# Kernel optimization log

Hardware: AMD Instinct MI355X
Metric: run time of the kernel (lower is better)

## Reference

```python
import jax, jax.numpy as jnp
import numpy as np

B, S, HID = 2, 2048, 3072
NH, NKV, HD = 16, 8, 256
N_REP = NH // NKV
BITS, BLK = 4, 128
THETA = 10000.0
NEG = -1e9


def quantize_bfp(x, bits=BITS, block_size=BLK):
    """Block-floating-point quantization: blocks of `block_size` along the last
    (head_dim) axis share one power-of-two exponent; mantissas get `bits` levels
    (sign + bits-1), round-to-nearest."""
    shape = x.shape
    xb = x.reshape(-1, block_size)
    maxabs = jnp.max(jnp.abs(xb), axis=-1, keepdims=True)
    e = jnp.floor(jnp.log2(jnp.maximum(maxabs, 1e-30)))
    scale = jnp.exp2(e - (bits - 2))  # largest mantissa ~ 2^(bits-1)-1 covers maxabs
    qmax = 2.0 ** (bits - 1) - 1.0
    q = jnp.clip(jnp.round(xb / scale), -qmax, qmax) * scale
    q = jnp.where(maxabs > 0, q, 0.0)
    return q.reshape(shape)


def rotate_half(x):
    x1, x2 = jnp.split(x, 2, axis=-1)
    return jnp.concatenate((-x2, x1), axis=-1)


def setup_inputs() -> dict:
    key = jax.random.key(0)
    ks = jax.random.split(key, 5)
    hidden_states = jax.random.normal(ks[0], (B, S, HID), dtype=jnp.float32)
    sd = 0.02
    Wq = jax.random.normal(ks[1], (NH * HD, HID), dtype=jnp.float32) * sd
    Wk = jax.random.normal(ks[2], (NKV * HD, HID), dtype=jnp.float32) * sd
    Wv = jax.random.normal(ks[3], (NKV * HD, HID), dtype=jnp.float32) * sd
    Wo = jax.random.normal(ks[4], (HID, NH * HD), dtype=jnp.float32) * sd
    # rotary tables (HF convention: concat(freqs, freqs))
    pos = jnp.arange(S, dtype=jnp.float32)
    inv_freq = 1.0 / (THETA ** (jnp.arange(0, HD, 2, dtype=jnp.float32) / HD))
    freqs = jnp.einsum('s,d->sd', pos, inv_freq)
    emb = jnp.concatenate((freqs, freqs), axis=-1)  # (S, HD)
    cos = jnp.cos(emb)[None]  # (1, S, HD)
    sin = jnp.sin(emb)[None]
    # additive causal mask (B, 1, S, S)
    causal = jnp.where(jnp.tril(jnp.ones((S, S), dtype=bool)), 0.0, NEG).astype(jnp.float32)
    attention_mask = jnp.broadcast_to(causal[None, None], (B, 1, S, S))
    return {"hidden_states": hidden_states, "Wq": Wq, "Wk": Wk, "Wv": Wv,
            "Wo": Wo, "cos": cos, "sin": sin, "attention_mask": attention_mask}


def reference(hidden_states, Wq, Wk, Wv, Wo, cos, sin, attention_mask):
    b, s, _ = hidden_states.shape
    q = jnp.einsum('bsh,dh->bsd', hidden_states, Wq).reshape(b, s, NH, HD).transpose(0, 2, 1, 3)
    k = jnp.einsum('bsh,dh->bsd', hidden_states, Wk).reshape(b, s, NKV, HD).transpose(0, 2, 1, 3)
    v = jnp.einsum('bsh,dh->bsd', hidden_states, Wv).reshape(b, s, NKV, HD).transpose(0, 2, 1, 3)
    # RoPE (cos/sin unsqueezed at dim 1 -> (1,1,S,HD))
    c, sn = cos[:, None], sin[:, None]
    q = q * c + rotate_half(q) * sn
    k = k * c + rotate_half(k) * sn
    # int4 BFP quantization of keys (along rows of head_dim)
    k = quantize_bfp(k)
    # GQA: repeat kv heads
    k = jnp.repeat(k, N_REP, axis=1)
    v = jnp.repeat(v, N_REP, axis=1)
    scores = jnp.einsum('bhqd,bhkd->bhqk', q, k) / jnp.sqrt(jnp.float32(HD))
    scores = scores + attention_mask
    attn = jax.nn.softmax(scores.astype(jnp.float32), axis=-1).astype(q.dtype)
    out = jnp.einsum('bhqk,bhkd->bhqd', attn, v)
    out = out.transpose(0, 2, 1, 3).reshape(b, s, NH * HD)
    return jnp.einsum('bsd,hd->bsh', out, Wo)
```

## Files before the change

kernel.cpp:

```cpp
#include <hip/hip_runtime.h>
#include <math.h>

#define Bsz 2
#define Ssz 2048
#define HIDs 3072
#define NHs 16
#define NKVs 8
#define HDs 256

typedef _Float16 f16;
typedef _Float16 f16x8 __attribute__((ext_vector_type(8)));
typedef _Float16 f16x4 __attribute__((ext_vector_type(4)));
typedef float f32x4 __attribute__((ext_vector_type(4)));

__device__ __forceinline__ void async16(const f16* g, f16* l) {
    __builtin_amdgcn_global_load_lds(
        (const __attribute__((address_space(1))) void*)g,
        (__attribute__((address_space(3))) void*)l, 16, 0, 0);
}

__device__ __forceinline__ float row_max16(float v) {
    int t;
    t = __builtin_amdgcn_mov_dpp(__float_as_int(v), 0x121, 0xf, 0xf, false);
    v = fmaxf(v, __int_as_float(t));
    t = __builtin_amdgcn_mov_dpp(__float_as_int(v), 0x122, 0xf, 0xf, false);
    v = fmaxf(v, __int_as_float(t));
    t = __builtin_amdgcn_mov_dpp(__float_as_int(v), 0x124, 0xf, 0xf, false);
    v = fmaxf(v, __int_as_float(t));
    t = __builtin_amdgcn_mov_dpp(__float_as_int(v), 0x128, 0xf, 0xf, false);
    v = fmaxf(v, __int_as_float(t));
    return v;
}
__device__ __forceinline__ float row_sum16(float v) {
    int t;
    t = __builtin_amdgcn_mov_dpp(__float_as_int(v), 0x121, 0xf, 0xf, false);
    v = v + __int_as_float(t);
    t = __builtin_amdgcn_mov_dpp(__float_as_int(v), 0x122, 0xf, 0xf, false);
    v = v + __int_as_float(t);
    t = __builtin_amdgcn_mov_dpp(__float_as_int(v), 0x124, 0xf, 0xf, false);
    v = v + __int_as_float(t);
    t = __builtin_amdgcn_mov_dpp(__float_as_int(v), 0x128, 0xf, 0xf, false);
    v = v + __int_as_float(t);
    return v;
}

__global__ void cast_f32_f16_v4(const float4* __restrict__ in, f16x4* __restrict__ out, int n4) {
    int i = blockIdx.x * blockDim.x + threadIdx.x;
    if (i < n4) {
        float4 v = in[i];
        f16x4 r;
        r[0] = (f16)v.x; r[1] = (f16)v.y; r[2] = (f16)v.z; r[3] = (f16)v.w;
        out[i] = r;
    }
}

__global__ __launch_bounds__(256) void gemm_nt_f16(
    const f16* __restrict__ A, const f16* __restrict__ Bm, float* __restrict__ C,
    int M, int N, int K)
{
    __shared__ __align__(16) f16 As[128 * 32];
    __shared__ __align__(16) f16 Bs[128 * 32];
    const int tid  = threadIdx.x;
    const int wave = tid >> 6, lane = tid & 63;
    const int l15  = lane & 15, quad = lane >> 4;
    const int m0 = blockIdx.y * 128, n0 = blockIdx.x * 128;
    const int wm = (wave >> 1) * 64, wn = (wave & 1) * 64;
    const int srow = wave * 32 + (lane >> 2);
    const int scol = (lane & 3) * 8;

    f32x4 acc[4][4];
    const f32x4 fz = {0.f, 0.f, 0.f, 0.f};
#pragma unroll
    for (int i = 0; i < 4; i++)
#pragma unroll
        for (int j = 0; j < 4; j++) acc[i][j] = fz;

    const f16* Ag0 = A  + (size_t)(m0 + srow) * K + scol;
    const f16* Ag1 = A  + (size_t)(m0 + srow + 16) * K + scol;
    const f16* Bg0 = Bm + (size_t)(n0 + srow) * K + scol;
    const f16* Bg1 = Bm + (size_t)(n0 + srow + 16) * K + scol;
    f16* Al0 = As + (wave * 32) * 32;
    f16* Al1 = As + (wave * 32 + 16) * 32;
    f16* Bl0 = Bs + (wave * 32) * 32;
    f16* Bl1 = Bs + (wave * 32 + 16) * 32;

    for (int k0 = 0; k0 < K; k0 += 32) {
        __syncthreads();
        async16(Ag0 + k0, Al0);
        async16(Ag1 + k0, Al1);
        async16(Bg0 + k0, Bl0);
        async16(Bg1 + k0, Bl1);
        __syncthreads();
        f16x8 af[4], bfr[4];
#pragma unroll
        for (int i = 0; i < 4; i++)
            af[i] = *(const f16x8*)(As + (wm + i * 16 + l15) * 32 + quad * 8);
#pragma unroll
        for (int j = 0; j < 4; j++)
            bfr[j] = *(const f16x8*)(Bs + (wn + j * 16 + l15) * 32 + quad * 8);
#pragma unroll
        for (int i = 0; i < 4; i++)
#pragma unroll
            for (int j = 0; j < 4; j++)
                acc[i][j] = __builtin_amdgcn_mfma_f32_16x16x32_f16(af[i], bfr[j], acc[i][j], 0, 0, 0);
    }
#pragma unroll
    for (int i = 0; i < 4; i++) {
        const int r = m0 + wm + i * 16 + quad * 4;
#pragma unroll
        for (int j = 0; j < 4; j++) {
            const int c = n0 + wn + j * 16 + l15;
#pragma unroll
            for (int rr = 0; rr < 4; rr++)
                C[(size_t)(r + rr) * N + c] = acc[i][j][rr];
        }
    }
}

__global__ void rope_q_kernel(const float* __restrict__ qp, const float* __restrict__ cosb,
                              const float* __restrict__ sinb, f16* __restrict__ qo) {
    const int s = blockIdx.x, h = blockIdx.y, b = blockIdx.z;
    const int d = threadIdx.x;
    const float* row = qp + (size_t)(b * Ssz + s) * (NHs * HDs) + h * HDs;
    float x = row[d];
    float other = (d < 128) ? -row[d + 128] : row[d - 128];
    float val = (x * cosb[s * HDs + d] + other * sinb[s * HDs + d]) * 0.0625f;
    qo[((size_t)(b * NHs + h) * Ssz + s) * HDs + d] = (f16)val;
}

__global__ void rope_quant_k_kernel(const float* __restrict__ kp, const float* __restrict__ cosb,
                                    const float* __restrict__ sinb, f16* __restrict__ ko) {
    const int s = blockIdx.x, h = blockIdx.y, b = blockIdx.z;
    const int d = threadIdx.x;
    const float* row = kp + (size_t)(b * Ssz + s) * (NKVs * HDs) + h * HDs;
    float x = row[d];
    float other = (d < 128) ? -row[d + 128] : row[d - 128];
    float val = x * cosb[s * HDs + d] + other * sinb[s * HDs + d];
    __shared__ float red[256];
    red[d] = fabsf(val);
    __syncthreads();
    for (int off = 64; off >= 1; off >>= 1) {
        if ((d & 127) < off) red[d] = fmaxf(red[d], red[d + off]);
        __syncthreads();
    }
    float maxabs = red[d & 128];
    float out;
    if (maxabs > 0.f) {
        int ex;
        frexpf(maxabs, &ex);
        float scale = ldexpf(1.0f, ex - 3);
        float q = rintf(val / scale);
        q = fminf(7.f, fmaxf(-7.f, q));
        out = q * scale;
    } else out = 0.f;
    ko[((size_t)(b * NKVs + h) * Ssz + s) * HDs + d] = (f16)out;
}

__global__ __launch_bounds__(256) void transpose_v_kernel(
    const float* __restrict__ proj, f16* __restrict__ vt)
{
    const int s0 = blockIdx.x * 64, c0 = blockIdx.y * 64, b = blockIdx.z;
    const int tid = threadIdx.x;
    __shared__ f16 T[64 * 72];
    {
        const int r = tid >> 2, cc = (tid & 3) * 16;
        const float* src = proj + (size_t)(b * Ssz + s0 + r) * (NKVs * HDs) + c0 + cc;
        f16 tmp[16];
#pragma unroll
        for (int q4 = 0; q4 < 4; q4++) {
            float4 v = *(const float4*)(src + q4 * 4);
            tmp[q4 * 4 + 0] = (f16)v.x; tmp[q4 * 4 + 1] = (f16)v.y;
            tmp[q4 * 4 + 2] = (f16)v.z; tmp[q4 * 4 + 3] = (f16)v.w;
        }
        *(f16x8*)(T + r * 72 + cc)     = *(f16x8*)(tmp);
        *(f16x8*)(T + r * 72 + cc + 8) = *(f16x8*)(tmp + 8);
    }
    __syncthreads();
    {
        const int d = tid >> 2, sc = (tid & 3) * 16;
        f16 tmp[16];
#pragma unroll
        for (int j = 0; j < 16; j++) tmp[j] = T[(sc + j) * 72 + d];
        const int col = c0 + d;
        const int kh = col >> 8, dd = col & 255;
        f16* dst = vt + ((size_t)(b * NKVs + kh) * HDs + dd) * Ssz + s0 + sc;
        *(f16x8*)(dst)     = *(f16x8*)(tmp);
        *(f16x8*)(dst + 8) = *(f16x8*)(tmp + 8);
    }
}

__global__ __launch_bounds__(256, 2) void attn_kernel(
    const f16* __restrict__ Q,
    const f16* __restrict__ Kq,
    const f16* __restrict__ Vt,
    f16* __restrict__ O)
{
    const int qt = (gridDim.x - 1) - blockIdx.x;
    const int h = blockIdx.y, b = blockIdx.z;
    const int kh = h >> 1;
    const int tid = threadIdx.x;
    const int wave = tid >> 6, lane = tid & 63;
    const int l15 = lane & 15, quad = lane >> 4;
    const int wrow = qt * 64 + wave * 16;

    const f16* Qb  = Q  + ((size_t)(b * NHs  + h)  * Ssz) * HDs;
    const f16* Kg  = Kq + ((size_t)(b * NKVs + kh) * Ssz) * HDs;
    const f16* Vtg = Vt + ((size_t)(b * NKVs + kh) * HDs) * Ssz;

    __shared__ __align__(16) f16 Ks[32 * 256];
    __shared__ __align__(16) f16 Vs[256 * 32];
    __shared__ __align__(16) f16 Pl[4 * 16 * 40];
    f16* Pw = Pl + wave * 16 * 40;

    const int k_r   = lane >> 5;
    const int k_cs  = (lane & 31) ^ (k_r << 2);
    const int v_r   = lane >> 2;
    const int v_c   = (lane & 3) * 8;

    f16x8 qf[8];
    {
        const f16* qrow = Qb + (size_t)(wrow + l15) * HDs + quad * 8;
#pragma unroll
        for (int ks = 0; ks < 8; ks++)
            qf[ks] = *(const f16x8*)(qrow + ks * 32);
    }

    const f32x4 fz = {0.f, 0.f, 0.f, 0.f};
    f32x4 accO[16];
#pragma unroll
    for (int jn = 0; jn < 16; jn++) accO[jn] = fz;
    float mrow[4], lpart[4];
#pragma unroll
    for (int r = 0; r < 4; r++) { mrow[r] = -1e30f; lpart[r] = 0.f; }

    const int nk = 2 * qt + 2;
    const int wave_max_row = wrow + 15;

    for (int kt = 0; kt < nk; kt++) {
        const int kvb = kt * 32;
        __syncthreads();
#pragma unroll
        for (int t = 0; t < 4; t++) {
            const int r2 = wave * 8 + t * 2;
            async16(Kg + (size_t)(kvb + r2 + k_r) * 256 + k_cs * 8, Ks + r2 * 256);
        }
#pragma unroll
        for (int t = 0; t < 4; t++) {
            const int d0 = wave * 64 + t * 16;
            async16(Vtg + (size_t)(d0 + v_r) * Ssz + kvb + v_c, Vs + d0 * 32);
        }
        __syncthreads();

        if (kvb <= wave_max_row) {
            f32x4 sv0 = fz, sv1 = fz;
            const int sw0 = (l15 & 1) << 2;
#pragma unroll
            for (int ks = 0; ks < 8; ks++) {
                const int cpos = ((ks * 4 + quad) ^ sw0) * 8;
                f16x8 kf0 = *(const f16x8*)(Ks + l15 * 256 + cpos);
                f16x8 kf1 = *(const f16x8*)(Ks + (16 + l15) * 256 + cpos);
                sv0 = __builtin_amdgcn_mfma_f32_16x16x32_f16(qf[ks], kf0, sv0, 0, 0, 0);
                sv1 = __builtin_amdgcn_mfma_f32_16x16x32_f16(qf[ks], kf1, sv1, 0, 0, 0);
            }
            float aup[4];
            bool need = false;
#pragma unroll
            for (int r = 0; r < 4; r++) {
                float s0 = sv0[r], s1 = sv1[r];
                const int row = wrow + quad * 4 + r;
                if (kvb + 31 > row) {
                    if (kvb + l15 > row)      s0 = -1e30f;
                    if (kvb + 16 + l15 > row) s1 = -1e30f;
                }
                float rmax = row_max16(fmaxf(s0, s1));
                float mold = mrow[r];
                float mnew = fmaxf(mold, rmax);
                aup[r] = __expf(mold - mnew);
                need = need || (mnew > mold);
                float p0 = __expf(s0 - mnew);
                float p1 = __expf(s1 - mnew);
                lpart[r] = lpart[r] * aup[r] + (p0 + p1);
                mrow[r] = mnew;
                Pw[(quad * 4 + r) * 40 + l15]      = (f16)p0;
                Pw[(quad * 4 + r) * 40 + 16 + l15] = (f16)p1;
            }
            if (__any(need)) {
#pragma unroll
                for (int jn = 0; jn < 16; jn++) {
                    f32x4 t = accO[jn];
                    t[0] *= aup[0]; t[1] *= aup[1]; t[2] *= aup[2]; t[3] *= aup[3];
                    accO[jn] = t;
                }
            }
            f16x8 pf = *(const f16x8*)(Pw + l15 * 40 + quad * 8);
#pragma unroll
            for (int jn = 0; jn < 16; jn++) {
                f16x8 vf = *(const f16x8*)(Vs + (jn * 16 + l15) * 32 + quad * 8);
                accO[jn] = __builtin_amdgcn_mfma_f32_16x16x32_f16(pf, vf, accO[jn], 0, 0, 0);
            }
        }
    }
#pragma unroll
    for (int r = 0; r < 4; r++) {
        const int row = wrow + quad * 4 + r;
        const float inv = 1.0f / row_sum16(lpart[r]);
        f16* orow = O + ((size_t)(b * Ssz) + row) * (NHs * HDs) + h * HDs;
#pragma unroll
        for (int jn = 0; jn < 16; jn++)
            orow[jn * 16 + l15] = (f16)(accO[jn][r] * inv);
    }
}

extern "C" void kernel_launch(void* const* d_in, const int* in_sizes, int n_in,
                              void* d_out, int out_size, void* d_ws, size_t ws_size,
                              hipStream_t stream) {
    const float* hs   = (const float*)d_in[0];
    const float* Wq   = (const float*)d_in[1];
    const float* Wk   = (const float*)d_in[2];
    const float* Wv   = (const float*)d_in[3];
    const float* Wo   = (const float*)d_in[4];
    const float* cosb = (const float*)d_in[5];
    const float* sinb = (const float*)d_in[6];
    float* out = (float*)d_out;

    char* ws = (char*)d_ws;
    f16*   hs_h = (f16*)(ws);
    f16*   w_h  = (f16*)(ws + 25165824);
    float* proj = (float*)(ws + 50331648);
    f16*   q_h  = (f16*)(ws + 117440512);
    f16*   k_h  = (f16*)(ws + 150994944);
    f16*   vt_h = (f16*)(ws + 167772160);
    f16*   ao_h = (f16*)proj;

    int n4;
    n4 = (Bsz * Ssz * HIDs) / 4;
    cast_f32_f16_v4<<<n4 / 256, 256, 0, stream>>>((const float4*)hs, (f16x4*)hs_h, n4);
    n4 = (NHs * HDs * HIDs) / 4;
    cast_f32_f16_v4<<<n4 / 256, 256, 0, stream>>>((const float4*)Wq, (f16x4*)w_h, n4);
    gemm_nt_f16<<<dim3(4096 / 128, 4096 / 128), 256, 0, stream>>>(hs_h, w_h, proj, 4096, 4096, 3072);
    rope_q_kernel<<<dim3(Ssz, NHs, Bsz), 256, 0, stream>>>(proj, cosb, sinb, q_h);
    n4 = (NKVs * HDs * HIDs) / 4;
    cast_f32_f16_v4<<<n4 / 256, 256, 0, stream>>>((const float4*)Wk, (f16x4*)w_h, n4);
    gemm_nt_f16<<<dim3(2048 / 128, 4096 / 128), 256, 0, stream>>>(hs_h, w_h, proj, 4096, 2048, 3072);
    rope_quant_k_kernel<<<dim3(Ssz, NKVs, Bsz), 256, 0, stream>>>(proj, cosb, sinb, k_h);
    n4 = (NKVs * HDs * HIDs) / 4;
    cast_f32_f16_v4<<<n4 / 256, 256, 0, stream>>>((const float4*)Wv, (f16x4*)w_h, n4);
    gemm_nt_f16<<<dim3(2048 / 128, 4096 / 128), 256, 0, stream>>>(hs_h, w_h, proj, 4096, 2048, 3072);
    transpose_v_kernel<<<dim3(Ssz / 64, (NKVs * HDs) / 64, Bsz), 256, 0, stream>>>(proj, vt_h);
    attn_kernel<<<dim3(Ssz / 64, NHs, Bsz), 256, 0, stream>>>(q_h, k_h, vt_h, ao_h);
    n4 = (HIDs * NHs * HDs) / 4;
    cast_f32_f16_v4<<<n4 / 256, 256, 0, stream>>>((const float4*)Wo, (f16x4*)w_h, n4);
    gemm_nt_f16<<<dim3(3072 / 128, 4096 / 128), 256, 0, stream>>>(ao_h, w_h, out, 4096, 3072, 4096);
}
```

Baseline: 1.021 ms.

## Merge weight casts into one launch and double per-wave query rows in attention

All five f32-to-f16 casts now run in a single kernel, writing the weights into separate buffers (reusing the q/k/vt buffers for Wq/Wk/Wv before they are overwritten). This removes several launches and keeps the Wo cast off the critical path. The attention kernel now handles 128 query rows per block, 32 per wave, so each K/V tile loaded into LDS is reused across twice as many query rows and the launch has half as many blocks. The V tile in LDS also gets an XOR swizzle to reduce bank conflicts. The cost is higher register pressure, with two sets of accumulators and Q fragments per wave, and less parallelism under the causal load imbalance.

Measured after the change: 1.003 ms. Within noise of the previous version (-1.7%).

```diff
diff --git a/kernel.cpp b/kernel.cpp
--- a/kernel.cpp
+++ b/kernel.cpp
@@ -44,14 +44,30 @@
     return v;
 }
 
-__global__ void cast_f32_f16_v4(const float4* __restrict__ in, f16x4* __restrict__ out, int n4) {
+#define N4_HS  3145728
+#define N4_WQ  3145728
+#define N4_WK  1572864
+#define N4_WV  1572864
+#define N4_WO  3145728
+#define N4_TOT (N4_HS + N4_WQ + N4_WK + N4_WV + N4_WO)
+
+__global__ void cast_all_kernel(const float4* __restrict__ hs, const float4* __restrict__ wq,
+                                const float4* __restrict__ wk, const float4* __restrict__ wv,
+                                const float4* __restrict__ wo,
+                                f16x4* __restrict__ hs_h, f16x4* __restrict__ wq_h,
+                                f16x4* __restrict__ wk_h, f16x4* __restrict__ wv_h,
+                                f16x4* __restrict__ wo_h) {
     int i = blockIdx.x * blockDim.x + threadIdx.x;
-    if (i < n4) {
-        float4 v = in[i];
-        f16x4 r;
-        r[0] = (f16)v.x; r[1] = (f16)v.y; r[2] = (f16)v.z; r[3] = (f16)v.w;
-        out[i] = r;
-    }
+    const float4* src; f16x4* dst; int off;
+    if (i < N4_HS)                       { src = hs; dst = hs_h; off = i; }
+    else if (i < N4_HS + N4_WQ)          { src = wq; dst = wq_h; off = i - N4_HS; }
+    else if (i < N4_HS + N4_WQ + N4_WK)  { src = wk; dst = wk_h; off = i - (N4_HS + N4_WQ); }
+    else if (i < N4_TOT - N4_WO)         { src = wv; dst = wv_h; off = i - (N4_HS + N4_WQ + N4_WK); }
+    else                                 { src = wo; dst = wo_h; off = i - (N4_TOT - N4_WO); }
+    float4 v = src[off];
+    f16x4 r;
+    r[0] = (f16)v.x; r[1] = (f16)v.y; r[2] = (f16)v.z; r[3] = (f16)v.w;
+    dst[off] = r;
 }
 
 __global__ __launch_bounds__(256) void gemm_nt_f16(
@@ -201,7 +217,7 @@
     const int tid = threadIdx.x;
     const int wave = tid >> 6, lane = tid & 63;
     const int l15 = lane & 15, quad = lane >> 4;
-    const int wrow = qt * 64 + wave * 16;
+    const int wrow = qt * 128 + wave * 32;
 
     const f16* Qb  = Q  + ((size_t)(b * NHs  + h)  * Ssz) * HDs;
     const f16* Kg  = Kq + ((size_t)(b * NKVs + kh) * Ssz) * HDs;
@@ -209,32 +225,35 @@
 
     __shared__ __align__(16) f16 Ks[32 * 256];
     __shared__ __align__(16) f16 Vs[256 * 32];
-    __shared__ __align__(16) f16 Pl[4 * 16 * 40];
-    f16* Pw = Pl + wave * 16 * 40;
-
-    const int k_r   = lane >> 5;
-    const int k_cs  = (lane & 31) ^ (k_r << 2);
-    const int v_r   = lane >> 2;
-    const int v_c   = (lane & 3) * 8;
-
-    f16x8 qf[8];
+    __shared__ __align__(16) f16 Pl[4 * 32 * 40];
+    f16* Pw = Pl + wave * 32 * 40;
+
+    const int k_r  = lane >> 5;
+    const int k_cs = (lane & 31) ^ (k_r << 2);
+    const int v_r  = lane >> 2;
+    const int v_cs = ((lane & 3) ^ (v_r & 3)) * 8;
+
+    f16x8 qf0[8], qf1[8];
     {
-        const f16* qrow = Qb + (size_t)(wrow + l15) * HDs + quad * 8;
-#pragma unroll
-        for (int ks = 0; ks < 8; ks++)
-            qf[ks] = *(const f16x8*)(qrow + ks * 32);
+        const f16* qrow0 = Qb + (size_t)(wrow + l15) * HDs + quad * 8;
+        const f16* qrow1 = qrow0 + (size_t)16 * HDs;
+#pragma unroll
+        for (int ks = 0; ks < 8; ks++) {
+            qf0[ks] = *(const f16x8*)(qrow0 + ks * 32);
+            qf1[ks] = *(const f16x8*)(qrow1 + ks * 32);
+        }
     }
 
     const f32x4 fz = {0.f, 0.f, 0.f, 0.f};
-    f32x4 accO[16];
-#pragma unroll
-    for (int jn = 0; jn < 16; jn++) accO[jn] = fz;
-    float mrow[4], lpart[4];
-#pragma unroll
-    for (int r = 0; r < 4; r++) { mrow[r] = -1e30f; lpart[r] = 0.f; }
-
-    const int nk = 2 * qt + 2;
-    const int wave_max_row = wrow + 15;
+    f32x4 accO0[16], accO1[16];
+#pragma unroll
+    for (int jn = 0; jn < 16; jn++) { accO0[jn] = fz; accO1[jn] = fz; }
+    float mrow0[4], mrow1[4], lp0[4], lp1[4];
+#pragma unroll
+    for (int r = 0; r < 4; r++) { mrow0[r] = -1e30f; mrow1[r] = -1e30f; lp0[r] = 0.f; lp1[r] = 0.f; }
+
+    const int nk = 4 * qt + 4;
+    const int wave_max_row = wrow + 31;
 
     for (int kt = 0; kt < nk; kt++) {
         const int kvb = kt * 32;
@@ -247,67 +266,96 @@
 #pragma unroll
         for (int t = 0; t < 4; t++) {
             const int d0 = wave * 64 + t * 16;
-            async16(Vtg + (size_t)(d0 + v_r) * Ssz + kvb + v_c, Vs + d0 * 32);
+            async16(Vtg + (size_t)(d0 + v_r) * Ssz + kvb + v_cs, Vs + d0 * 32);
         }
         __syncthreads();
 
         if (kvb <= wave_max_row) {
-            f32x4 sv0 = fz, sv1 = fz;
+            f32x4 s00 = fz, s01 = fz, s10 = fz, s11 = fz;
             const int sw0 = (l15 & 1) << 2;
 #pragma unroll
             for (int ks = 0; ks < 8; ks++) {
                 const int cpos = ((ks * 4 + quad) ^ sw0) * 8;
                 f16x8 kf0 = *(const f16x8*)(Ks + l15 * 256 + cpos);
                 f16x8 kf1 = *(const f16x8*)(Ks + (16 + l15) * 256 + cpos);
-                sv0 = __builtin_amdgcn_mfma_f32_16x16x32_f16(qf[ks], kf0, sv0, 0, 0, 0);
-                sv1 = __builtin_amdgcn_mfma_f32_16x16x32_f16(qf[ks], kf1, sv1, 0, 0, 0);
+                s00 = __builtin_amdgcn_mfma_f32_16x16x32_f16(qf0[ks], kf0, s00, 0, 0, 0);
+                s01 = __builtin_amdgcn_mfma_f32_16x16x32_f16(qf0[ks], kf1, s01, 0, 0, 0);
+                s10 = __builtin_amdgcn_mfma_f32_16x16x32_f16(qf1[ks], kf0, s10, 0, 0, 0);
+                s11 = __builtin_amdgcn_mfma_f32_16x16x32_f16(qf1[ks], kf1, s11, 0, 0, 0);
             }
-            float aup[4];
+            float a0[4], a1[4];
             bool need = false;
+            const bool diag = (kvb + 31 > wrow);
 #pragma unroll
             for (int r = 0; r < 4; r++) {
-                float s0 = sv0[r], s1 = sv1[r];
-                const int row = wrow + quad * 4 + r;
-                if (kvb + 31 > row) {
-                    if (kvb + l15 > row)      s0 = -1e30f;
-                    if (kvb + 16 + l15 > row) s1 = -1e30f;
+                float x0 = s00[r], x1 = s01[r];
+                const int row0 = wrow + quad * 4 + r;
+                if (diag) {
+                    if (kvb + l15 > row0)      x0 = -1e30f;
+                    if (kvb + 16 + l15 > row0) x1 = -1e30f;
                 }
-                float rmax = row_max16(fmaxf(s0, s1));
-                float mold = mrow[r];
+                float rmax = row_max16(fmaxf(x0, x1));
+                float mold = mrow0[r];
                 float mnew = fmaxf(mold, rmax);
-                aup[r] = __expf(mold - mnew);
+                a0[r] = __expf(mold - mnew);
                 need = need || (mnew > mold);
-                float p0 = __expf(s0 - mnew);
-                float p1 = __expf(s1 - mnew);
-                lpart[r] = lpart[r] * aup[r] + (p0 + p1);
-                mrow[r] = mnew;
+                float p0 = __expf(x0 - mnew);
+                float p1 = __expf(x1 - mnew);
+                lp0[r] = lp0[r] * a0[r] + (p0 + p1);
+                mrow0[r] = mnew;
                 Pw[(quad * 4 + r) * 40 + l15]      = (f16)p0;
                 Pw[(quad * 4 + r) * 40 + 16 + l15] = (f16)p1;
+                float y0 = s10[r], y1 = s11[r];
+                const int row1 = row0 + 16;
+                if (diag) {
+                    if (kvb + l15 > row1)      y0 = -1e30f;
+                    if (kvb + 16 + l15 > row1) y1 = -1e30f;
+                }
+                float rmax1 = row_max16(fmaxf(y0, y1));
+                float mold1 = mrow1[r];
+                float mnew1 = fmaxf(mold1, rmax1);
+                a1[r] = __expf(mold1 - mnew1);
+                need = need || (mnew1 > mold1);
+                float q0 = __expf(y0 - mnew1);
+                float q1 = __expf(y1 - mnew1);
+                lp1[r] = lp1[r] * a1[r] + (q0 + q1);
+                mrow1[r] = mnew1;
+                Pw[(16 + quad * 4 + r) * 40 + l15]      = (f16)q0;
+                Pw[(16 + quad * 4 + r) * 40 + 16 + l15] = (f16)q1;
             }
             if (__any(need)) {
 #pragma unroll
                 for (int jn = 0; jn < 16; jn++) {
-                    f32x4 t = accO[jn];
-                    t[0] *= aup[0]; t[1] *= aup[1]; t[2] *= aup[2]; t[3] *= aup[3];
-                    accO[jn] = t;
+                    f32x4 t0 = accO0[jn], t1 = accO1[jn];
+                    t0[0] *= a0[0]; t0[1] *= a0[1]; t0[2] *= a0[2]; t0[3] *= a0[3];
+                    t1[0] *= a1[0]; t1[1] *= a1[1]; t1[2] *= a1[2]; t1[3] *= a1[3];
+                    accO0[jn] = t0; accO1[jn] = t1;
                 }
             }
-            f16x8 pf = *(const f16x8*)(Pw + l15 * 40 + quad * 8);
+            f16x8 pf0 = *(const f16x8*)(Pw + l15 * 40 + quad * 8);
+            f16x8 pf1 = *(const f16x8*)(Pw + (16 + l15) * 40 + quad * 8);
 #pragma unroll
             for (int jn = 0; jn < 16; jn++) {
-                f16x8 vf = *(const f16x8*)(Vs + (jn * 16 + l15) * 32 + quad * 8);
-                accO[jn] = __builtin_amdgcn_mfma_f32_16x16x32_f16(pf, vf, accO[jn], 0, 0, 0);
+                f16x8 vf = *(const f16x8*)(Vs + (jn * 16 + l15) * 32 + ((quad ^ (l15 & 3))) * 8);
+                accO0[jn] = __builtin_amdgcn_mfma_f32_16x16x32_f16(pf0, vf, accO0[jn], 0, 0, 0);
+                accO1[jn] = __builtin_amdgcn_mfma_f32_16x16x32_f16(pf1, vf, accO1[jn], 0, 0, 0);
             }
         }
     }
 #pragma unroll
     for (int r = 0; r < 4; r++) {
-        const int row = wrow + quad * 4 + r;
-        const float inv = 1.0f / row_sum16(lpart[r]);
-        f16* orow = O + ((size_t)(b * Ssz) + row) * (NHs * HDs) + h * HDs;
+        const int row0 = wrow + quad * 4 + r;
+        const float inv0 = 1.0f / row_sum16(lp0[r]);
+        f16* orow0 = O + ((size_t)(b * Ssz) + row0) * (NHs * HDs) + h * HDs;
 #pragma unroll
         for (int jn = 0; jn < 16; jn++)
-            orow[jn * 16 + l15] = (f16)(accO[jn][r] * inv);
+            orow0[jn * 16 + l15] = (f16)(accO0[jn][r] * inv0);
+        const int row1 = row0 + 16;
+        const float inv1 = 1.0f / row_sum16(lp1[r]);
+        f16* orow1 = O + ((size_t)(b * Ssz) + row1) * (NHs * HDs) + h * HDs;
+#pragma unroll
+        for (int jn = 0; jn < 16; jn++)
+            orow1[jn * 16 + l15] = (f16)(accO1[jn][r] * inv1);
     }
 }
 
@@ -325,30 +373,24 @@
 
     char* ws = (char*)d_ws;
     f16*   hs_h = (f16*)(ws);
-    f16*   w_h  = (f16*)(ws + 25165824);
+    f16*   wo_h = (f16*)(ws + 25165824);
     float* proj = (float*)(ws + 50331648);
     f16*   q_h  = (f16*)(ws + 117440512);
     f16*   k_h  = (f16*)(ws + 150994944);
     f16*   vt_h = (f16*)(ws + 167772160);
     f16*   ao_h = (f16*)proj;
 
-    int n4;
-    n4 = (Bsz * Ssz * HIDs) / 4;
-    cast_f32_f16_v4<<<n4 / 256, 256, 0, stream>>>((const float4*)hs, (f16x4*)hs_h, n4);
-    n4 = (NHs * HDs * HIDs) / 4;
-    cast_f32_f16_v4<<<n4 / 256, 256, 0, stream>>>((const float4*)Wq, (f16x4*)w_h, n4);
-    gemm_nt_f16<<<dim3(4096 / 128, 4096 / 128), 256, 0, stream>>>(hs_h, w_h, proj, 4096, 4096, 3072);
+    cast_all_kernel<<<N4_TOT / 256, 256, 0, stream>>>(
+        (const float4*)hs, (const float4*)Wq, (const float4*)Wk,
+        (const float4*)Wv, (const float4*)Wo,
+        (f16x4*)hs_h, (f16x4*)q_h, (f16x4*)k_h, (f16x4*)vt_h, (f16x4*)wo_h);
+
+    gemm_nt_f16<<<dim3(4096 / 128, 4096 / 128), 256, 0, stream>>>(hs_h, q_h, proj, 4096, 4096, 3072);
     rope_q_kernel<<<dim3(Ssz, NHs, Bsz), 256, 0, stream>>>(proj, cosb, sinb, q_h);
-    n4 = (NKVs * HDs * HIDs) / 4;
-    cast_f32_f16_v4<<<n4 / 256, 256, 0, stream>>>((const float4*)Wk, (f16x4*)w_h, n4);
-    gemm_nt_f16<<<dim3(2048 / 128, 4096 / 128), 256, 0, stream>>>(hs_h, w_h, proj, 4096, 2048, 3072);
+    gemm_nt_f16<<<dim3(2048 / 128, 4096 / 128), 256, 0, stream>>>(hs_h, k_h, proj, 4096, 2048, 3072);
     rope_quant_k_kernel<<<dim3(Ssz, NKVs, Bsz), 256, 0, stream>>>(proj, cosb, sinb, k_h);
-    n4 = (NKVs * HDs * HIDs) / 4;
-    cast_f32_f16_v4<<<n4 / 256, 256, 0, stream>>>((const float4*)Wv, (f16x4*)w_h, n4);
-    gemm_nt_f16<<<dim3(2048 / 128, 4096 / 128), 256, 0, stream>>>(hs_h, w_h, proj, 4096, 2048, 3072);
+    gemm_nt_f16<<<dim3(2048 / 128, 4096 / 128), 256, 0, stream>>>(hs_h, vt_h, proj, 4096, 2048, 3072);
     transpose_v_kernel<<<dim3(Ssz / 64, (NKVs * HDs) / 64, Bsz), 256, 0, stream>>>(proj, vt_h);
-    attn_kernel<<<dim3(Ssz / 64, NHs, Bsz), 256, 0, stream>>>(q_h, k_h, vt_h, ao_h);
-    n4 = (HIDs * NHs * HDs) / 4;
-    cast_f32_f16_v4<<<n4 / 256, 256, 0, stream>>>((const float4*)Wo, (f16x4*)w_h, n4);
-    gemm_nt_f16<<<dim3(3072 / 128, 4096 / 128), 256, 0, stream>>>(ao_h, w_h, out, 4096, 3072, 4096);
-}
+    attn_kernel<<<dim3(Ssz / 128, NHs, Bsz), 256, 0, stream>>>(q_h, k_h, vt_h, ao_h);
+    gemm_nt_f16<<<dim3(3072 / 128, 4096 / 128), 256, 0, stream>>>(ao_h, wo_h, out, 4096, 3072, 4096);
+}
```
